# Performance work log

Hardware: AMD Instinct MI355X
Metric: run time of the kernel (lower is better)

## Reference

```python
import jax, jax.numpy as jnp
import numpy as np
from jax.scipy.linalg import cho_solve

N = 4096        # num nodes
D = 256         # in_dim == out_dim
NUM_HOPS = 2
R = 32          # subspace_dim
ETA = 0.5
EPS_SUB = 0.5   # eps in coeff = r / (n * eps^2)
LN_EPS = 1e-5


def setup_inputs() -> dict:
    rng = np.random.default_rng(0)
    K = NUM_HOPS + 1
    # sparse-ish binary adjacency mask with self loops
    mask = (rng.random((N, N)) < 0.002).astype(np.float32)
    mask = np.maximum(mask, np.eye(N, dtype=np.float32))
    deg = mask.sum(axis=1, keepdims=True)
    A = (mask / deg).astype(np.float32)          # row-stochastic propagation
    L = (np.eye(N, dtype=np.float32) - A)        # normalized Laplacian
    H = rng.standard_normal((N, D)).astype(np.float32)
    # orthonormal subspace bases per hop, as in __init__ (QR of randn)
    U = np.stack([np.linalg.qr(rng.standard_normal((D, R)))[0][:, :R] for _ in range(K)]).astype(np.float32)
    lambda_laps = np.full((K,), 0.1, dtype=np.float32)
    hop_weights = np.full((K,), 1.0 / K, dtype=np.float32)
    threshold = np.full((D,), 0.05, dtype=np.float32)
    gamma = np.ones((D,), dtype=np.float32)
    beta = np.zeros((D,), dtype=np.float32)
    return {
        "H": jnp.asarray(H), "A": jnp.asarray(A), "adj_mask": jnp.asarray(mask),
        "L": jnp.asarray(L), "U": jnp.asarray(U),
        "lambda_laps": jnp.asarray(lambda_laps), "hop_weights": jnp.asarray(hop_weights),
        "threshold": jnp.asarray(threshold), "gamma": jnp.asarray(gamma), "beta": jnp.asarray(beta),
    }


def reference(H, A, adj_mask, L, U, lambda_laps, hop_weights, threshold, gamma, beta):
    n, d = H.shape
    r = U.shape[-1]
    # multi-hop propagation
    hops = [H]
    Hk = H
    for _ in range(NUM_HOPS):
        Hk = A @ Hk
        hops.append(Hk)
    w = jax.nn.softmax(hop_weights)
    laps = jax.nn.softplus(lambda_laps)
    coeff = r / (n * EPS_SUB ** 2)
    neg = (1.0 - adj_mask) * -1e9
    I_r = jnp.eye(r, dtype=H.dtype)
    agg = jnp.zeros_like(H)        # accumulates grad_k.T, shape [n, d]
    lap_total = jnp.zeros_like(H)
    for k, H_k in enumerate(hops):
        Uk = U[k]                  # [d, r]
        Zk = Uk.T @ H_k.T          # [r, n]
        M = I_r + coeff * (Zk @ Zk.T)              # [r, r], SPD
        Lc = jnp.linalg.cholesky(M)
        M_inv = cho_solve((Lc, True), I_r)         # cholesky_inverse
        MZ = M_inv @ Zk                            # [r, n]
        scores = Zk.T @ MZ + neg                   # [n, n] masked subspace attention
        alpha = jax.nn.softmax(scores, axis=1)
        grad_k = (Uk @ (MZ @ alpha.T)).T           # [n, d]
        agg = agg + w[k] * grad_k
        lap_total = lap_total + laps[k] * (L @ H_k)
    H_half = H + ETA * agg - ETA * lap_total
    # soft-threshold (proj is None since in_dim == out_dim)
    H_out = jnp.sign(H_half) * jax.nn.relu(jnp.abs(H_half) - threshold[None, :])
    H_out = H_out + H              # residual
    mu = H_out.mean(axis=-1, keepdims=True)
    var = H_out.var(axis=-1, keepdims=True)
    H_out = (H_out - mu) / jnp.sqrt(var + LN_EPS) * gamma + beta
    # orthogonality loss over all (k, l) pairs
    K = U.shape[0]
    orth_loss = jnp.asarray(0.0, dtype=H.dtype)
    for k in range(K):
        for l in range(k, K):
            G = U[k].T @ U[l]
            orth_loss = orth_loss + jnp.sum(((G - I_r) if l == k else G) ** 2)
    lap_smooth = jnp.sum(H_out * (L @ H_out))  # trace(H^T L H)
    return H_out, orth_loss, lap_smooth, jax.lax.stop_gradient(w)
```

## Files before the change

### kernel.cpp

```cpp
#include <hip/hip_runtime.h>
#include <math.h>

#define NN 4096
#define DD 256
#define KK 3
#define RR 32
#define MAXNNZ 128

static constexpr float ETA    = 0.5f;
static constexpr float COEFF  = 0.03125f;
static constexpr float LN_EPSF = 1e-5f;

#define OFF_H1   0
#define OFF_H2   (NN*DD)
#define OFF_H3   (2*NN*DD)
#define OFF_Y    (3*NN*DD)
#define OFF_P    (OFF_Y + KK*NN*RR)
#define OFF_M    (OFF_P + KK*NN*RR)
#define OFF_MINV (OFF_M + KK*RR*RR)
#define OFF_SCAL (OFF_MINV + KK*RR*RR)
#define OFF_NNZ  (OFF_SCAL + 8)
#define OFF_COLS (OFF_NNZ + NN)
#define OFF_VALS (OFF_COLS + NN*MAXNNZ)
#define OFF_PART (OFF_VALS + NN*MAXNNZ)
#define OFF_ORTH (OFF_PART + NN/4)

__global__ void k_csr_prep(const float* __restrict__ A, int* __restrict__ nnz,
                           int* __restrict__ cols, float* __restrict__ vals,
                           const float* __restrict__ hw, const float* __restrict__ ll,
                           const float* __restrict__ U,
                           float* __restrict__ ws, float* __restrict__ out) {
  int b = blockIdx.x;
  int t = threadIdx.x;
  if (b >= NN) {
    int p = b - NN;
    if (p == 6) {
      if (t == 0) {
        float m = fmaxf(fmaxf(hw[0], hw[1]), hw[2]);
        float e0 = expf(hw[0]-m), e1 = expf(hw[1]-m), e2 = expf(hw[2]-m);
        float s = e0 + e1 + e2;
        float w0 = e0/s, w1 = e1/s, w2 = e2/s;
        ws[OFF_SCAL+0] = w0; ws[OFF_SCAL+1] = w1; ws[OFF_SCAL+2] = w2;
        for (int k = 0; k < KK; ++k) {
          float x = ll[k];
          ws[OFF_SCAL+3+k] = (x > 20.f) ? x : log1pf(expf(x));
        }
        out[NN*DD + 2] = w0; out[NN*DD + 3] = w1; out[NN*DD + 4] = w2;
      }
      for (int idx = t; idx < KK*RR*RR; idx += 256) {
        int rr2 = idx % (RR*RR);
        ws[OFF_M + idx] = ((rr2 / RR) == (rr2 % RR)) ? 1.f : 0.f;
      }
      return;
    }
    int k = (p < 3) ? 0 : ((p < 5) ? 1 : 2);
    int l = (p < 3) ? p : ((p < 5) ? p - 2 : 2);
    int a0 = t >> 5, bb = t & 31;
    float s0 = 0.f, s1 = 0.f, s2 = 0.f, s3 = 0.f;
    for (int dd = 0; dd < DD; ++dd) {
      float ul = U[(size_t)l*DD*RR + dd*RR + bb];
      const float* uk = U + (size_t)k*DD*RR + dd*RR;
      s0 += uk[a0]      * ul;
      s1 += uk[a0 + 8]  * ul;
      s2 += uk[a0 + 16] * ul;
      s3 += uk[a0 + 24] * ul;
    }
    if (k == l && bb == a0)      s0 -= 1.f;
    if (k == l && bb == a0 + 8)  s1 -= 1.f;
    if (k == l && bb == a0 + 16) s2 -= 1.f;
    if (k == l && bb == a0 + 24) s3 -= 1.f;
    float sq = s0*s0 + s1*s1 + s2*s2 + s3*s3;
    #pragma unroll
    for (int o = 32; o > 0; o >>= 1) sq += __shfl_xor(sq, o, 64);
    __shared__ float red[4];
    if ((t & 63) == 0) red[t >> 6] = sq;
    __syncthreads();
    if (t == 0) ws[OFF_ORTH + p] = red[0] + red[1] + red[2] + red[3];
    return;
  }
  int i = b;
  __shared__ int cnt;
  if (t == 0) cnt = 0;
  __syncthreads();
  const float4* row4 = (const float4*)(A + (size_t)i * NN);
  for (int j0 = 0; j0 < NN/4; j0 += 256) {
    float4 v = row4[j0 + t];
    int jb = (j0 + t) * 4;
    if (v.x != 0.f) { int p = atomicAdd(&cnt,1); if (p<MAXNNZ){cols[i*MAXNNZ+p]=jb+0; vals[i*MAXNNZ+p]=v.x;} }
    if (v.y != 0.f) { int p = atomicAdd(&cnt,1); if (p<MAXNNZ){cols[i*MAXNNZ+p]=jb+1; vals[i*MAXNNZ+p]=v.y;} }
    if (v.z != 0.f) { int p = atomicAdd(&cnt,1); if (p<MAXNNZ){cols[i*MAXNNZ+p]=jb+2; vals[i*MAXNNZ+p]=v.z;} }
    if (v.w != 0.f) { int p = atomicAdd(&cnt,1); if (p<MAXNNZ){cols[i*MAXNNZ+p]=jb+3; vals[i*MAXNNZ+p]=v.w;} }
  }
  __syncthreads();
  int n = cnt < MAXNNZ ? cnt : MAXNNZ;
  int npad = (n + 7) & ~7;
  for (int e = n + t; e < npad; e += 256) {
    cols[i*MAXNNZ + e] = i;
    vals[i*MAXNNZ + e] = 0.f;
  }
  if (t == 0) nnz[i] = n;
}

__global__ void k_spmvy(const float* __restrict__ X, float* __restrict__ Hout,
                        const int* __restrict__ nnz, const int* __restrict__ cols,
                        const float* __restrict__ vals,
                        const float* __restrict__ Uo, float* __restrict__ Yo,
                        const float* __restrict__ Un, float* __restrict__ Yn) {
  int t = threadIdx.x;
  int r = t >> 6, lane = t & 63;
  int row = blockIdx.x * 4 + r;
  int d4 = lane * 4;
  int n = nnz[row];
  int npad = (n + 7) & ~7;
  const int* ci = cols + row*MAXNNZ;
  const float* vi = vals + row*MAXNNZ;
  float4 acc = {0.f, 0.f, 0.f, 0.f};
  float4 own = {0.f, 0.f, 0.f, 0.f};
  for (int e0 = 0; e0 < npad; e0 += 8) {
    int4 c0 = *(const int4*)(ci + e0);
    int4 c1 = *(const int4*)(ci + e0 + 4);
    float4 v0 = *(const float4*)(vi + e0);
    float4 v1 = *(const float4*)(vi + e0 + 4);
    float4 x0 = *(const float4*)(X + (size_t)c0.x*DD + d4);
    float4 x1 = *(const float4*)(X + (size_t)c0.y*DD + d4);
    float4 x2 = *(const float4*)(X + (size_t)c0.z*DD + d4);
    float4 x3 = *(const float4*)(X + (size_t)c0.w*DD + d4);
    float4 x4 = *(const float4*)(X + (size_t)c1.x*DD + d4);
    float4 x5 = *(const float4*)(X + (size_t)c1.y*DD + d4);
    float4 x6 = *(const float4*)(X + (size_t)c1.z*DD + d4);
    float4 x7 = *(const float4*)(X + (size_t)c1.w*DD + d4);
    if (c0.x == row) own = x0;
    if (c0.y == row) own = x1;
    if (c0.z == row) own = x2;
    if (c0.w == row) own = x3;
    if (c1.x == row) own = x4;
    if (c1.y == row) own = x5;
    if (c1.z == row) own = x6;
    if (c1.w == row) own = x7;
    acc.x += v0.x*x0.x + v0.y*x1.x + v0.z*x2.x + v0.w*x3.x + v1.x*x4.x + v1.y*x5.x + v1.z*x6.x + v1.w*x7.x;
    acc.y += v0.x*x0.y + v0.y*x1.y + v0.z*x2.y + v0.w*x3.y + v1.x*x4.y + v1.y*x5.y + v1.z*x6.y + v1.w*x7.y;
    acc.z += v0.x*x0.z + v0.y*x1.z + v0.z*x2.z + v0.w*x3.z + v1.x*x4.z + v1.y*x5.z + v1.z*x6.z + v1.w*x7.z;
    acc.w += v0.x*x0.w + v0.y*x1.w + v0.z*x2.w + v0.w*x3.w + v1.x*x4.w + v1.y*x5.w + v1.z*x6.w + v1.w*x7.w;
  }
  *(float4*)(Hout + (size_t)row*DD + d4) = acc;
  if (!Uo && !Un) return;
  __shared__ float Hs[4][2][DD];
  *(float4*)&Hs[r][0][d4] = own;
  *(float4*)&Hs[r][1][d4] = acc;
  __syncthreads();
  int c = lane & 31, h = lane >> 5;
  if (Uo) {
    float part = 0.f;
    #pragma unroll 8
    for (int d = h*128; d < h*128 + 128; ++d) part += Hs[r][0][d] * Uo[d*RR + c];
    part += __shfl_xor(part, 32, 64);
    if (h == 0) Yo[(size_t)row*RR + c] = part;
  }
  if (Un) {
    float part = 0.f;
    #pragma unroll 8
    for (int d = h*128; d < h*128 + 128; ++d) part += Hs[r][1][d] * Un[d*RR + c];
    part += __shfl_xor(part, 32, 64);
    if (h == 0) Yn[(size_t)row*RR + c] = part;
  }
}

__global__ __launch_bounds__(1024) void k_gram(const float* __restrict__ Y, float* __restrict__ M) {
  int k = blockIdx.y;
  __shared__ float Ys[128*RR];
  int t = threadIdx.x;
  const float* Yk = Y + (size_t)k*NN*RR + (size_t)blockIdx.x*128*RR;
  for (int idx = t; idx < 128*RR; idx += 1024) Ys[idx] = Yk[idx];
  __syncthreads();
  int a = t >> 5, b = t & 31;
  float s = 0.f;
  for (int i = 0; i < 128; ++i) s += Ys[i*RR + a] * Ys[i*RR + b];
  atomicAdd(&M[k*RR*RR + a*RR + b], COEFF * s);
}

__global__ __launch_bounds__(256) void k_gj(const float* __restrict__ M, float* __restrict__ Minv) {
  int k = blockIdx.x;
  __shared__ float B[RR][2*RR];
  int t = threadIdx.x;
  for (int idx = t; idx < RR*2*RR; idx += 256) {
    int r = idx >> 6, c = idx & 63;
    B[r][c] = (c < RR) ? M[k*RR*RR + r*RR + c] : ((c - RR == r) ? 1.f : 0.f);
  }
  __syncthreads();
  int c = t & 63, r0 = t >> 6;
  for (int j = 0; j < RR; ++j) {
    float bjc = B[j][c];
    float pinv = 1.f / B[j][j];
    float f[8];
    #pragma unroll
    for (int q = 0; q < 8; ++q) f[q] = B[r0 + 4*q][j];
    __syncthreads();
    float pb = pinv * bjc;
    #pragma unroll
    for (int q = 0; q < 8; ++q) {
      int r = r0 + 4*q;
      B[r][c] = (r == j) ? pb : (B[r][c] - f[q] * pb);
    }
    __syncthreads();
  }
  for (int idx = t; idx < RR*RR; idx += 256)
    Minv[k*RR*RR + (idx >> 5)*RR + (idx & 31)] = B[idx >> 5][RR + (idx & 31)];
}

__global__ void k_attn(const float* __restrict__ Y, const float* __restrict__ Minv,
                       float* __restrict__ P, const int* __restrict__ nnz,
                       const int* __restrict__ cols) {
  int i = blockIdx.x, k = blockIdx.y;
  int t = threadIdx.x;
  const float* Yk = Y + (size_t)k*NN*RR;
  __shared__ float Mi[RR*RR];
  __shared__ float Yi[RR];
  __shared__ float qv[RR];
  __shared__ float sc[MAXNNZ];
  __shared__ float vsum[RR];
  for (int idx = t; idx < RR*RR; idx += 64) Mi[idx] = Minv[k*RR*RR + idx];
  if (t < RR) Yi[t] = Yk[(size_t)i*RR + t];
  sc[t] = -1e30f; sc[t+64] = -1e30f;
  __syncthreads();
  if (t < RR) {
    float s = 0.f;
    #pragma unroll 8
    for (int a = 0; a < RR; ++a) s += Mi[a*RR + t] * Yi[a];
    qv[t] = s;
  }
  __syncthreads();
  int n = nnz[i], npad = (n + 7) & ~7;
  const int* ci = cols + i*MAXNNZ;
  for (int e = t; e < npad; e += 64) {
    const float4* yr = (const float4*)(Yk + (size_t)ci[e]*RR);
    float s = 0.f;
    #pragma unroll
    for (int qq = 0; qq < 8; ++qq) {
      float4 yv = yr[qq];
      s += yv.x*qv[4*qq] + yv.y*qv[4*qq+1] + yv.z*qv[4*qq+2] + yv.w*qv[4*qq+3];
    }
    sc[e] = (e < n) ? s : -1e30f;
  }
  __syncthreads();
  float s0 = sc[t], s1 = sc[t+64];
  float m = fmaxf(s0, s1);
  #pragma unroll
  for (int o = 32; o > 0; o >>= 1) m = fmaxf(m, __shfl_xor(m, o, 64));
  float e0v = expf(s0 - m), e1v = expf(s1 - m);
  sc[t] = e0v; sc[t+64] = e1v;
  float l = e0v + e1v;
  #pragma unroll
  for (int o = 32; o > 0; o >>= 1) l += __shfl_xor(l, o, 64);
  float linv = 1.f / l;
  __syncthreads();
  int c = t & 31, h = t >> 5;
  float acc = 0.f;
  for (int e = h; e < npad; e += 2) acc += sc[e] * Yk[(size_t)ci[e]*RR + c];
  acc += __shfl_xor(acc, 32, 64);
  if (t < RR) vsum[t] = acc * linv;
  __syncthreads();
  if (t < RR) {
    float s = 0.f;
    #pragma unroll 8
    for (int a = 0; a < RR; ++a) s += Mi[a*RR + t] * vsum[a];
    P[(size_t)k*NN*RR + (size_t)i*RR + t] = s;
  }
}

__global__ void k_epi(const float* __restrict__ H0, const float* __restrict__ ws,
                      const float* __restrict__ U, const float* __restrict__ thr,
                      const float* __restrict__ gma, const float* __restrict__ bta,
                      float* __restrict__ out) {
  __shared__ float Us[DD][RR+1];
  __shared__ float Ps[8][KK*RR];
  int t = threadIdx.x;
  int ty = t >> 5, tx = t & 31;
  int row0 = blockIdx.x * 8;
  const float* P    = ws + OFF_P;
  const float* scal = ws + OFF_SCAL;
  for (int idx = t; idx < 8*KK*RR; idx += 256) {
    int rl = idx / (KK*RR), kr = idx % (KK*RR);
    int k = kr / RR, rr2 = kr % RR;
    Ps[rl][kr] = P[(size_t)k*NN*RR + (size_t)(row0+rl)*RR + rr2];
  }
  float lp0 = scal[3], lp1 = scal[4], lp2 = scal[5];
  float gacc[8];
  #pragma unroll
  for (int j = 0; j < 8; ++j) gacc[j] = 0.f;
  for (int k = 0; k < KK; ++k) {
    __syncthreads();
    for (int idx = t; idx < DD*RR; idx += 256) Us[idx >> 5][idx & 31] = U[(size_t)k*DD*RR + idx];
    __syncthreads();
    float wk = scal[k];
    #pragma unroll
    for (int j = 0; j < 8; ++j) {
      int d = tx + 32*j;
      float s = 0.f;
      #pragma unroll
      for (int rr2 = 0; rr2 < RR; ++rr2) s += Ps[ty][k*RR + rr2] * Us[d][rr2];
      gacc[j] += wk * s;
    }
  }
  int i = row0 + ty;
  const float* H1 = ws + OFF_H1;
  const float* H2 = ws + OFF_H2;
  const float* H3 = ws + OFF_H3;
  float v[8]; float sum = 0.f, sumsq = 0.f;
  #pragma unroll
  for (int j = 0; j < 8; ++j) {
    int d = tx + 32*j;
    size_t idx = (size_t)i*DD + d;
    float h0 = H0[idx], h1 = H1[idx], h2 = H2[idx], h3 = H3[idx];
    float lap = lp0*(h0-h1) + lp1*(h1-h2) + lp2*(h2-h3);
    float hf = h0 + ETA*gacc[j] - ETA*lap;
    float a = fabsf(hf) - thr[d];
    float sft = (a > 0.f) ? copysignf(a, hf) : 0.f;
    float x = sft + h0;
    v[j] = x; sum += x; sumsq += x*x;
  }
  #pragma unroll
  for (int o = 16; o > 0; o >>= 1) {
    sum   += __shfl_xor(sum, o, 32);
    sumsq += __shfl_xor(sumsq, o, 32);
  }
  float mu  = sum * (1.f/DD);
  float var = sumsq * (1.f/DD) - mu*mu;
  float inv = rsqrtf(var + LN_EPSF);
  #pragma unroll
  for (int j = 0; j < 8; ++j) {
    int d = tx + 32*j;
    out[(size_t)i*DD + d] = (v[j] - mu) * inv * gma[d] + bta[d];
  }
}

__global__ void k_lapsm(const float* __restrict__ Hout, const int* __restrict__ nnz,
                        const int* __restrict__ cols, const float* __restrict__ vals,
                        float* __restrict__ partial) {
  int t = threadIdx.x;
  int row = blockIdx.x * 4 + (t >> 6);
  int d4 = (t & 63) * 4;
  int n = nnz[row];
  int npad = (n + 7) & ~7;
  const int* ci = cols + row*MAXNNZ;
  const float* vi = vals + row*MAXNNZ;
  float4 acc = {0.f, 0.f, 0.f, 0.f};
  for (int e0 = 0; e0 < npad; e0 += 8) {
    int4 c0 = *(const int4*)(ci + e0);
    int4 c1 = *(const int4*)(ci + e0 + 4);
    float4 v0 = *(const float4*)(vi + e0);
    float4 v1 = *(const float4*)(vi + e0 + 4);
    float4 x0 = *(const float4*)(Hout + (size_t)c0.x*DD + d4);
    float4 x1 = *(const float4*)(Hout + (size_t)c0.y*DD + d4);
    float4 x2 = *(const float4*)(Hout + (size_t)c0.z*DD + d4);
    float4 x3 = *(const float4*)(Hout + (size_t)c0.w*DD + d4);
    float4 x4 = *(const float4*)(Hout + (size_t)c1.x*DD + d4);
    float4 x5 = *(const float4*)(Hout + (size_t)c1.y*DD + d4);
    float4 x6 = *(const float4*)(Hout + (size_t)c1.z*DD + d4);
    float4 x7 = *(const float4*)(Hout + (size_t)c1.w*DD + d4);
    acc.x += v0.x*x0.x + v0.y*x1.x + v0.z*x2.x + v0.w*x3.x + v1.x*x4.x + v1.y*x5.x + v1.z*x6.x + v1.w*x7.x;
    acc.y += v0.x*x0.y + v0.y*x1.y + v0.z*x2.y + v0.w*x3.y + v1.x*x4.y + v1.y*x5.y + v1.z*x6.y + v1.w*x7.y;
    acc.z += v0.x*x0.z + v0.y*x1.z + v0.z*x2.z + v0.w*x3.z + v1.x*x4.z + v1.y*x5.z + v1.z*x6.z + v1.w*x7.z;
    acc.w += v0.x*x0.w + v0.y*x1.w + v0.z*x2.w + v0.w*x3.w + v1.x*x4.w + v1.y*x5.w + v1.z*x6.w + v1.w*x7.w;
  }
  float4 h = *(const float4*)(Hout + (size_t)row*DD + d4);
  float part = h.x*(h.x-acc.x) + h.y*(h.y-acc.y) + h.z*(h.z-acc.z) + h.w*(h.w-acc.w);
  #pragma unroll
  for (int o = 32; o > 0; o >>= 1) part += __shfl_xor(part, o, 64);
  __shared__ float red[4];
  if ((t & 63) == 0) red[t >> 6] = part;
  __syncthreads();
  if (t == 0) partial[blockIdx.x] = red[0] + red[1] + red[2] + red[3];
}

__global__ void k_red(const float* __restrict__ ws, float* __restrict__ out) {
  const float* partial = ws + OFF_PART;
  int t = threadIdx.x;
  float4 p = *(const float4*)(partial + t*4);
  float s = p.x + p.y + p.z + p.w;
  #pragma unroll
  for (int o = 32; o > 0; o >>= 1) s += __shfl_xor(s, o, 64);
  __shared__ float red[4];
  if ((t & 63) == 0) red[t >> 6] = s;
  __syncthreads();
  if (t == 0) {
    out[1] = red[0] + red[1] + red[2] + red[3];
    const float* op = ws + OFF_ORTH;
    out[0] = op[0] + op[1] + op[2] + op[3] + op[4] + op[5];
  }
}

extern "C" void kernel_launch(void* const* d_in, const int* in_sizes, int n_in,
                              void* d_out, int out_size, void* d_ws, size_t ws_size,
                              hipStream_t stream) {
  const float* H   = (const float*)d_in[0];
  const float* A   = (const float*)d_in[1];
  const float* U   = (const float*)d_in[4];
  const float* ll  = (const float*)d_in[5];
  const float* hw  = (const float*)d_in[6];
  const float* thr = (const float*)d_in[7];
  const float* gma = (const float*)d_in[8];
  const float* bta = (const float*)d_in[9];
  float* out = (float*)d_out;
  float* ws  = (float*)d_ws;
  int* nnz   = (int*)(ws + OFF_NNZ);
  int* cols  = (int*)(ws + OFF_COLS);
  float* vals = ws + OFF_VALS;
  float* Y = ws + OFF_Y;

  k_csr_prep<<<NN + 7, 256, 0, stream>>>(A, nnz, cols, vals, hw, ll, U, ws, out);
  k_spmvy<<<NN/4, 256, 0, stream>>>(H, ws + OFF_H1, nnz, cols, vals,
                                    U, Y, U + (size_t)DD*RR, Y + (size_t)NN*RR);
  k_spmvy<<<NN/4, 256, 0, stream>>>(ws + OFF_H1, ws + OFF_H2, nnz, cols, vals,
                                    nullptr, nullptr, U + (size_t)2*DD*RR, Y + (size_t)2*NN*RR);
  k_spmvy<<<NN/4, 256, 0, stream>>>(ws + OFF_H2, ws + OFF_H3, nnz, cols, vals,
                                    nullptr, nullptr, nullptr, nullptr);
  dim3 g32(NN/128, KK);
  k_gram<<<g32, 1024, 0, stream>>>(Y, ws + OFF_M);
  k_gj<<<KK, 256, 0, stream>>>(ws + OFF_M, ws + OFF_MINV);
  dim3 gattn(NN, KK);
  k_attn<<<gattn, 64, 0, stream>>>(Y, ws + OFF_MINV, ws + OFF_P, nnz, cols);
  k_epi<<<NN/8, 256, 0, stream>>>(H, ws, U, thr, gma, bta, out);
  k_lapsm<<<NN/4, 256, 0, stream>>>(out, nnz, cols, vals, ws + OFF_PART);
  k_red<<<1, 256, 0, stream>>>(ws, out + NN*DD);
}
```

Before: 295.4 us.

## Fuse third hop SpMV into epilogue, fold Minv into U, batch attention rows

Drops the separate third SpMV kernel and computes A·H2 inside the epilogue, so the H3 buffer is never written and read back. Precomputes W = U·Minv in the Gauss-Jordan kernel, which removes the per-row Minv matvec from the attention kernel. The attention kernel now handles four rows per 256-thread block instead of one row per 64-thread block. The cost is a heavier epilogue, which does a gather over neighbors while holding more registers, and a serial 3-block W computation.

```diff
diff --git a/kernel.cpp b/kernel.cpp
--- a/kernel.cpp
+++ b/kernel.cpp
@@ -14,6 +14,7 @@
 #define OFF_H1   0
 #define OFF_H2   (NN*DD)
 #define OFF_H3   (2*NN*DD)
+#define OFF_W    OFF_H3
 #define OFF_Y    (3*NN*DD)
 #define OFF_P    (OFF_Y + KK*NN*RR)
 #define OFF_M    (OFF_P + KK*NN*RR)
@@ -178,7 +179,8 @@
   atomicAdd(&M[k*RR*RR + a*RR + b], COEFF * s);
 }
 
-__global__ __launch_bounds__(256) void k_gj(const float* __restrict__ M, float* __restrict__ Minv) {
+__global__ __launch_bounds__(256) void k_gj(const float* __restrict__ M, float* __restrict__ Minv,
+                                            const float* __restrict__ U, float* __restrict__ W) {
   int k = blockIdx.x;
   __shared__ float B[RR][2*RR];
   int t = threadIdx.x;
@@ -205,79 +207,103 @@
   }
   for (int idx = t; idx < RR*RR; idx += 256)
     Minv[k*RR*RR + (idx >> 5)*RR + (idx & 31)] = B[idx >> 5][RR + (idx & 31)];
-}
-
-__global__ void k_attn(const float* __restrict__ Y, const float* __restrict__ Minv,
+  for (int idx = t; idx < DD*RR; idx += 256) {
+    int d = idx >> 5, rr2 = idx & 31;
+    const float* ud = U + (size_t)k*DD*RR + (size_t)d*RR;
+    float s = 0.f;
+    #pragma unroll 8
+    for (int a = 0; a < RR; ++a) s += ud[a] * B[a][RR + rr2];
+    W[(size_t)k*DD*RR + idx] = s;
+  }
+}
+
+__global__ __launch_bounds__(256) void k_attn(const float* __restrict__ Y, const float* __restrict__ Minv,
                        float* __restrict__ P, const int* __restrict__ nnz,
                        const int* __restrict__ cols) {
-  int i = blockIdx.x, k = blockIdx.y;
-  int t = threadIdx.x;
+  int k = blockIdx.y;
+  int t = threadIdx.x;
+  int w = t >> 6, lane = t & 63;
+  int i = blockIdx.x * 4 + w;
   const float* Yk = Y + (size_t)k*NN*RR;
   __shared__ float Mi[RR*RR];
-  __shared__ float Yi[RR];
-  __shared__ float qv[RR];
-  __shared__ float sc[MAXNNZ];
-  __shared__ float vsum[RR];
-  for (int idx = t; idx < RR*RR; idx += 64) Mi[idx] = Minv[k*RR*RR + idx];
-  if (t < RR) Yi[t] = Yk[(size_t)i*RR + t];
-  sc[t] = -1e30f; sc[t+64] = -1e30f;
-  __syncthreads();
-  if (t < RR) {
+  __shared__ float Yi[4][RR];
+  __shared__ float qv[4][RR];
+  __shared__ float sc[4][MAXNNZ];
+  for (int idx = t; idx < RR*RR; idx += 256) Mi[idx] = Minv[k*RR*RR + idx];
+  if (lane < RR) Yi[w][lane] = Yk[(size_t)i*RR + lane];
+  sc[w][lane] = -1e30f; sc[w][lane+64] = -1e30f;
+  __syncthreads();
+  if (lane < RR) {
     float s = 0.f;
     #pragma unroll 8
-    for (int a = 0; a < RR; ++a) s += Mi[a*RR + t] * Yi[a];
-    qv[t] = s;
+    for (int a = 0; a < RR; ++a) s += Mi[a*RR + lane] * Yi[w][a];
+    qv[w][lane] = s;
   }
   __syncthreads();
   int n = nnz[i], npad = (n + 7) & ~7;
   const int* ci = cols + i*MAXNNZ;
-  for (int e = t; e < npad; e += 64) {
+  for (int e = lane; e < npad; e += 64) {
     const float4* yr = (const float4*)(Yk + (size_t)ci[e]*RR);
     float s = 0.f;
     #pragma unroll
     for (int qq = 0; qq < 8; ++qq) {
       float4 yv = yr[qq];
-      s += yv.x*qv[4*qq] + yv.y*qv[4*qq+1] + yv.z*qv[4*qq+2] + yv.w*qv[4*qq+3];
-    }
-    sc[e] = (e < n) ? s : -1e30f;
-  }
-  __syncthreads();
-  float s0 = sc[t], s1 = sc[t+64];
+      s += yv.x*qv[w][4*qq] + yv.y*qv[w][4*qq+1] + yv.z*qv[w][4*qq+2] + yv.w*qv[w][4*qq+3];
+    }
+    sc[w][e] = (e < n) ? s : -1e30f;
+  }
+  __syncthreads();
+  float s0 = sc[w][lane], s1 = sc[w][lane+64];
   float m = fmaxf(s0, s1);
   #pragma unroll
   for (int o = 32; o > 0; o >>= 1) m = fmaxf(m, __shfl_xor(m, o, 64));
   float e0v = expf(s0 - m), e1v = expf(s1 - m);
-  sc[t] = e0v; sc[t+64] = e1v;
+  sc[w][lane] = e0v; sc[w][lane+64] = e1v;
   float l = e0v + e1v;
   #pragma unroll
   for (int o = 32; o > 0; o >>= 1) l += __shfl_xor(l, o, 64);
   float linv = 1.f / l;
   __syncthreads();
-  int c = t & 31, h = t >> 5;
+  int c = lane & 31, h = lane >> 5;
   float acc = 0.f;
-  for (int e = h; e < npad; e += 2) acc += sc[e] * Yk[(size_t)ci[e]*RR + c];
+  for (int e = h; e < npad; e += 2) acc += sc[w][e] * Yk[(size_t)ci[e]*RR + c];
   acc += __shfl_xor(acc, 32, 64);
-  if (t < RR) vsum[t] = acc * linv;
-  __syncthreads();
-  if (t < RR) {
-    float s = 0.f;
-    #pragma unroll 8
-    for (int a = 0; a < RR; ++a) s += Mi[a*RR + t] * vsum[a];
-    P[(size_t)k*NN*RR + (size_t)i*RR + t] = s;
-  }
+  if (lane < RR) P[(size_t)k*NN*RR + (size_t)i*RR + lane] = acc * linv;
 }
 
 __global__ void k_epi(const float* __restrict__ H0, const float* __restrict__ ws,
-                      const float* __restrict__ U, const float* __restrict__ thr,
+                      const float* __restrict__ thr,
                       const float* __restrict__ gma, const float* __restrict__ bta,
+                      const int* __restrict__ nnz, const int* __restrict__ cols,
+                      const float* __restrict__ vals,
                       float* __restrict__ out) {
   __shared__ float Us[DD][RR+1];
   __shared__ float Ps[8][KK*RR];
   int t = threadIdx.x;
   int ty = t >> 5, tx = t & 31;
   int row0 = blockIdx.x * 8;
+  int i = row0 + ty;
   const float* P    = ws + OFF_P;
   const float* scal = ws + OFF_SCAL;
+  const float* W    = ws + OFF_W;
+  const float* H1   = ws + OFF_H1;
+  const float* H2   = ws + OFF_H2;
+  float h3a[8];
+  #pragma unroll
+  for (int j = 0; j < 8; ++j) h3a[j] = 0.f;
+  {
+    int n = nnz[i], npad = (n + 7) & ~7;
+    const int* ci = cols + (size_t)i*MAXNNZ;
+    const float* vi = vals + (size_t)i*MAXNNZ;
+    for (int e = 0; e < npad; e += 2) {
+      int ca = ci[e], cb = ci[e+1];
+      float va = vi[e], vb = vi[e+1];
+      const float* ra = H2 + (size_t)ca*DD + tx;
+      const float* rb = H2 + (size_t)cb*DD + tx;
+      #pragma unroll
+      for (int j = 0; j < 8; ++j) h3a[j] += va * ra[32*j] + vb * rb[32*j];
+    }
+  }
   for (int idx = t; idx < 8*KK*RR; idx += 256) {
     int rl = idx / (KK*RR), kr = idx % (KK*RR);
     int k = kr / RR, rr2 = kr % RR;
@@ -289,7 +315,7 @@
   for (int j = 0; j < 8; ++j) gacc[j] = 0.f;
   for (int k = 0; k < KK; ++k) {
     __syncthreads();
-    for (int idx = t; idx < DD*RR; idx += 256) Us[idx >> 5][idx & 31] = U[(size_t)k*DD*RR + idx];
+    for (int idx = t; idx < DD*RR; idx += 256) Us[idx >> 5][idx & 31] = W[(size_t)k*DD*RR + idx];
     __syncthreads();
     float wk = scal[k];
     #pragma unroll
@@ -301,17 +327,13 @@
       gacc[j] += wk * s;
     }
   }
-  int i = row0 + ty;
-  const float* H1 = ws + OFF_H1;
-  const float* H2 = ws + OFF_H2;
-  const float* H3 = ws + OFF_H3;
   float v[8]; float sum = 0.f, sumsq = 0.f;
   #pragma unroll
   for (int j = 0; j < 8; ++j) {
     int d = tx + 32*j;
     size_t idx = (size_t)i*DD + d;
-    float h0 = H0[idx], h1 = H1[idx], h2 = H2[idx], h3 = H3[idx];
-    float lap = lp0*(h0-h1) + lp1*(h1-h2) + lp2*(h2-h3);
+    float h0 = H0[idx], h1 = H1[idx], h2 = H2[idx];
+    float lap = lp0*(h0-h1) + lp1*(h1-h2) + lp2*(h2-h3a[j]);
     float hf = h0 + ETA*gacc[j] - ETA*lap;
     float a = fabsf(hf) - thr[d];
     float sft = (a > 0.f) ? copysignf(a, hf) : 0.f;
@@ -412,14 +434,12 @@
                                     U, Y, U + (size_t)DD*RR, Y + (size_t)NN*RR);
   k_spmvy<<<NN/4, 256, 0, stream>>>(ws + OFF_H1, ws + OFF_H2, nnz, cols, vals,
                                     nullptr, nullptr, U + (size_t)2*DD*RR, Y + (size_t)2*NN*RR);
-  k_spmvy<<<NN/4, 256, 0, stream>>>(ws + OFF_H2, ws + OFF_H3, nnz, cols, vals,
-                                    nullptr, nullptr, nullptr, nullptr);
   dim3 g32(NN/128, KK);
   k_gram<<<g32, 1024, 0, stream>>>(Y, ws + OFF_M);
-  k_gj<<<KK, 256, 0, stream>>>(ws + OFF_M, ws + OFF_MINV);
-  dim3 gattn(NN, KK);
-  k_attn<<<gattn, 64, 0, stream>>>(Y, ws + OFF_MINV, ws + OFF_P, nnz, cols);
-  k_epi<<<NN/8, 256, 0, stream>>>(H, ws, U, thr, gma, bta, out);
+  k_gj<<<KK, 256, 0, stream>>>(ws + OFF_M, ws + OFF_MINV, U, ws + OFF_W);
+  dim3 gattn(NN/4, KK);
+  k_attn<<<gattn, 256, 0, stream>>>(Y, ws + OFF_MINV, ws + OFF_P, nnz, cols);
+  k_epi<<<NN/8, 256, 0, stream>>>(H, ws, thr, gma, bta, nnz, cols, vals, out);
   k_lapsm<<<NN/4, 256, 0, stream>>>(out, nnz, cols, vals, ws + OFF_PART);
   k_red<<<1, 256, 0, stream>>>(ws, out + NN*DD);
 }
```

Result: slower. 313.6 us (+6.2%).
